# Performance work log

Measured on AMD Instinct MI355X. Metric: run time of the kernel, lower is better.

Reference implementation:

```python
import jax, jax.numpy as jnp
import numpy as np
from jax import lax

DIM = 1024
INNER = 2048  # dim * expand_factor
STATE = 64
B, T = 4, 2048
DECAY = 0.95
INPUT_FACTOR = 0.05
LN_EPS = 1e-5


def setup_inputs() -> dict:
    key = jax.random.key(0)
    ks = jax.random.split(key, 8)
    s = 0.02  # small weight scale
    return {
        "x": jax.random.normal(ks[0], (B, T, DIM), jnp.float32),
        "W_in": jax.random.normal(ks[1], (2 * INNER, DIM), jnp.float32) * s,
        "conv_w": jax.random.normal(ks[2], (INNER, 1, 4), jnp.float32) * s,
        "conv_b": jax.random.normal(ks[3], (INNER,), jnp.float32) * s,
        "W_B": jax.random.normal(ks[4], (STATE, INNER), jnp.float32) * s,
        "W_C": jax.random.normal(ks[5], (INNER, STATE), jnp.float32) * s,
        "D_param": jax.random.normal(ks[6], (INNER,), jnp.float32) * s,
        "W_out": jax.random.normal(ks[7], (DIM, INNER), jnp.float32) * s,
        "ln_gamma": jnp.ones((DIM,), jnp.float32),
        "ln_beta": jnp.zeros((DIM,), jnp.float32),
    }


def _layernorm(x, g, b):
    mu = jnp.mean(x, axis=-1, keepdims=True)
    var = jnp.mean(jnp.square(x - mu), axis=-1, keepdims=True)
    return (x - mu) * lax.rsqrt(var + LN_EPS) * g + b


def reference(x, W_in, conv_w, conv_b, W_B, W_C, D_param, W_out, ln_gamma, ln_beta):
    Bn, Tn, Dn = x.shape
    # in_proj -> split into input/gate halves
    x_proj = jnp.einsum("btd,ed->bte", x, W_in)  # [B,T,2*INNER]
    x_input, x_gate = jnp.split(x_proj, 2, axis=-1)
    # depthwise causal conv1d (torch pad=3 then slice [:T] == left-pad 3)
    xc = lax.conv_general_dilated(
        x_input.transpose(0, 2, 1),  # [B,C,T]
        conv_w,                       # [C,1,4]
        window_strides=(1,),
        padding=[(3, 0)],
        feature_group_count=INNER,
    ) + conv_b[None, :, None]
    u = jax.nn.silu(xc).transpose(0, 2, 1)  # [B,T,INNER]
    # linear recurrence: h_t = 0.95*h_{t-1} + 0.05*B_proj(u_t); h_0 = 0
    Bu = jnp.einsum("btc,sc->bts", u, W_B)  # [B,T,STATE]

    def step(h, bu_t):
        h = DECAY * h + INPUT_FACTOR * bu_t
        return h, h

    h0 = jnp.zeros((Bn, STATE), x.dtype)
    _, hs = lax.scan(step, h0, Bu.transpose(1, 0, 2))  # hs: [T,B,STATE]
    hs = hs.transpose(1, 0, 2)  # [B,T,STATE]
    y = jnp.einsum("bts,cs->btc", hs, W_C) + D_param * u  # [B,T,INNER]
    y = y * jax.nn.silu(x_gate)
    y = jnp.einsum("btc,dc->btd", y, W_out)  # [B,T,DIM]
    return _layernorm(y + x, ln_gamma, ln_beta)
```

## Files before the change

kernel.cpp:

```cpp
#include <hip/hip_runtime.h>
#include <hip/hip_bf16.h>

#define T_SEQ 2048
#define DIMD  1024
#define INNER 2048
#define STATE 64
#define BATCH 4
#define NCHUNK 64
#define CHUNK_L (T_SEQ / NCHUNK)
#define MROWS (BATCH * T_SEQ)
#define PSTRIDE ((long)MROWS * STATE)

typedef __hip_bfloat16 bf16;
typedef __attribute__((ext_vector_type(8))) short bf16x8v;
typedef __attribute__((ext_vector_type(4))) float f32x4v;
typedef __attribute__((ext_vector_type(4))) short short4v;

__device__ __forceinline__ float b2f(short s) {
    unsigned u = ((unsigned)(unsigned short)s) << 16;
    float f;
    __builtin_memcpy(&f, &u, 4);
    return f;
}
__device__ __forceinline__ short f2b(float f) {
    bf16 h = __float2bfloat16(f);
    short s;
    __builtin_memcpy(&s, &h, 2);
    return s;
}

__device__ __forceinline__ void gld_lds16(void* lds, const void* gsrc) {
    __builtin_amdgcn_global_load_lds(
        (const __attribute__((address_space(1))) unsigned*)gsrc,
        (__attribute__((address_space(3))) unsigned*)lds, 16, 0, 0);
}

template<int N> __device__ __forceinline__ void waitcnt_vm() {
    if constexpr (N == 8)      asm volatile("s_waitcnt vmcnt(8)" ::: "memory");
    else if constexpr (N == 4) asm volatile("s_waitcnt vmcnt(4)" ::: "memory");
    else                       asm volatile("s_waitcnt vmcnt(0)" ::: "memory");
}
__device__ __forceinline__ void block_barrier() {
    asm volatile("" ::: "memory");
    __builtin_amdgcn_s_barrier();
    asm volatile("" ::: "memory");
}

template<int BM, int BN, int BK, int WR, int WC, int EPI, int SPLITK>
__global__ __launch_bounds__(WR*WC*64, 2)
void gemm_ring(const short* __restrict__ A, const short* __restrict__ B,
               void* __restrict__ Cout, int M, int N, int K,
               const short* __restrict__ u_ptr, const short* __restrict__ gate_ptr,
               const float* __restrict__ Dp)
{
    constexpr int MFR = BM / (WR * 16);
    constexpr int NFR = BN / (WC * 16);
    constexpr int THREADS = WR * WC * 64;
    constexpr int UPR = BK / 8;
    constexpr int AISS = (BM * UPR) / THREADS;
    constexpr int BISS = (BN * UPR) / THREADS;
    constexpr int LPS  = AISS + BISS;
    __shared__ __align__(16) short As[2][BM * BK];
    __shared__ __align__(16) short Bs[2][BN * BK];

    const int tid  = threadIdx.x;
    const int lane = tid & 63;
    const int wave = tid >> 6;
    const int wm = (wave / WC) * (MFR * 16);
    const int wn = (wave % WC) * (NFR * 16);
    const long bm = (long)blockIdx.y * BM;
    const long bn = (long)blockIdx.x * BN;

    f32x4v acc[MFR][NFR];
#pragma unroll
    for (int m = 0; m < MFR; m++)
#pragma unroll
        for (int n = 0; n < NFR; n++)
            acc[m][n] = (f32x4v){0.f, 0.f, 0.f, 0.f};

    const int rsel = lane & 15;
    const int ssrc = (((tid & 7) ^ ((tid >> 3) & 7)) * 8);
    const int swz  = lane & 7;

    int kbeg = 0, kend = K;
    if constexpr (SPLITK > 1) {
        const int kch = K / SPLITK;
        kbeg = blockIdx.z * kch;
        kend = kbeg + kch;
    }
    const int nt = (kend - kbeg) / BK;

    auto stage = [&](int buf, int k0) {
#pragma unroll
        for (int i = 0; i < AISS; i++) {
            const int j = i * THREADS + tid;
            gld_lds16(&As[buf][j * 8],
                      &A[(bm + (j >> 3)) * (long)K + k0 + ssrc]);
        }
#pragma unroll
        for (int i = 0; i < BISS; i++) {
            const int j = i * THREADS + tid;
            gld_lds16(&Bs[buf][j * 8],
                      &B[(bn + (j >> 3)) * (long)K + k0 + ssrc]);
        }
    };
    auto compute = [&](int buf) {
#pragma unroll
        for (int kk = 0; kk < BK; kk += 32) {
            const int slog = (kk >> 3) + (lane >> 4);
            const int soff = ((slog ^ swz) * 8);
            bf16x8v af[MFR], bfv[NFR];
#pragma unroll
            for (int m = 0; m < MFR; m++)
                af[m] = *(const bf16x8v*)&As[buf][(wm + m * 16 + rsel) * BK + soff];
#pragma unroll
            for (int n = 0; n < NFR; n++)
                bfv[n] = *(const bf16x8v*)&Bs[buf][(wn + n * 16 + rsel) * BK + soff];
#pragma unroll
            for (int m = 0; m < MFR; m++)
#pragma unroll
                for (int n = 0; n < NFR; n++)
                    acc[m][n] = __builtin_amdgcn_mfma_f32_16x16x32_bf16(
                        af[m], bfv[n], acc[m][n], 0, 0, 0);
        }
    };

    stage(0, kbeg);
    for (int t = 0; t < nt; ++t) {
        const bool pf = (t + 1 < nt);
        if (pf) stage((t + 1) & 1, kbeg + (t + 1) * BK);
        if (pf) waitcnt_vm<LPS>();
        else    waitcnt_vm<0>();
        block_barrier();
        compute(t & 1);
        block_barrier();
    }

    float* fout = (float*)Cout;
    if constexpr (SPLITK > 1)
        fout += (long)blockIdx.z * (long)M * N;

#pragma unroll
    for (int m = 0; m < MFR; m++) {
#pragma unroll
        for (int n = 0; n < NFR; n++) {
            const long col  = bn + wn + n * 16 + (lane & 15);
            const long row0 = bm + wm + m * 16 + (lane >> 4) * 4;
#pragma unroll
            for (int j = 0; j < 4; j++) {
                const long row = row0 + j;
                const float v = acc[m][n][j];
                const long idx = row * (long)N + col;
                if constexpr (EPI == 0) {
                    ((short*)Cout)[idx] = f2b(v);
                } else if constexpr (EPI == 1) {
                    fout[idx] = v;
                } else {
                    float uv = b2f(u_ptr[row * (long)INNER + col]);
                    float gv = b2f(gate_ptr[row * (long)(2 * INNER) + col]);
                    float yv = v + Dp[col] * uv;
                    float sg = gv / (1.f + __expf(-gv));
                    ((short*)Cout)[idx] = f2b(yv * sg);
                }
            }
        }
    }
}

__global__ __launch_bounds__(256)
void conv_silu_kernel(const short* __restrict__ xproj, const float* __restrict__ cw,
                      const float* __restrict__ cb, short* __restrict__ u)
{
    const int bt = blockIdx.x;
    const int t  = bt & (T_SEQ - 1);
    const int c0 = threadIdx.x * 8;

    float wreg[4][8];
#pragma unroll
    for (int i = 0; i < 8; i++) {
        float4 wv = *(const float4*)&cw[(c0 + i) * 4];
        wreg[0][i] = wv.x; wreg[1][i] = wv.y; wreg[2][i] = wv.z; wreg[3][i] = wv.w;
    }
    float acc[8];
#pragma unroll
    for (int i = 0; i < 8; i++) acc[i] = cb[c0 + i];

#pragma unroll
    for (int k = 0; k < 4; k++) {
        if (t - 3 + k < 0) continue;
        bf16x8v v = *(const bf16x8v*)&xproj[(long)(bt - 3 + k) * (2 * INNER) + c0];
#pragma unroll
        for (int i = 0; i < 8; i++) acc[i] += b2f(v[i]) * wreg[k][i];
    }
    short o[8];
#pragma unroll
    for (int i = 0; i < 8; i++) {
        float s = acc[i] / (1.f + __expf(-acc[i]));
        o[i] = f2b(s);
    }
    *(bf16x8v*)&u[(long)bt * INNER + c0] = *(const bf16x8v*)o;
}

__global__ __launch_bounds__(64)
void scan_local_kernel(const float* __restrict__ Bu, float* __restrict__ locfin)
{
    const int b  = blockIdx.x / NCHUNK;
    const int ch = blockIdx.x % NCHUNK;
    const long base = ((long)b * T_SEQ + (long)ch * CHUNK_L) * STATE + threadIdx.x;
    float h = 0.f;
#pragma unroll
    for (int t = 0; t < CHUNK_L; t++) {
        const long o = base + (long)t * STATE;
        float bu = (Bu[o] + Bu[o + PSTRIDE]) + (Bu[o + 2 * PSTRIDE] + Bu[o + 3 * PSTRIDE]);
        h = 0.95f * h + 0.05f * bu;
    }
    locfin[(long)blockIdx.x * STATE + threadIdx.x] = h;
}

__global__ __launch_bounds__(256)
void carry_kernel(const float* __restrict__ locfin, float* __restrict__ carry,
                  float decayL)
{
    __shared__ float sm[BATCH * NCHUNK * STATE];
    for (int i = threadIdx.x; i < BATCH * NCHUNK * STATE; i += 256)
        sm[i] = locfin[i];
    __syncthreads();
    const int b = threadIdx.x >> 6, s = threadIdx.x & 63;
    float c = 0.f;
    for (int ch = 0; ch < NCHUNK; ch++) {
        const int idx = (b * NCHUNK + ch) * STATE + s;
        carry[idx] = c;
        c = decayL * c + sm[idx];
    }
}

__global__ __launch_bounds__(64)
void scan_apply_kernel(const float* __restrict__ Bu, const float* __restrict__ carry,
                       short* __restrict__ hs)
{
    const int b  = blockIdx.x / NCHUNK;
    const int ch = blockIdx.x % NCHUNK;
    const long base = ((long)b * T_SEQ + (long)ch * CHUNK_L) * STATE + threadIdx.x;
    float h = carry[(long)blockIdx.x * STATE + threadIdx.x];
#pragma unroll
    for (int t = 0; t < CHUNK_L; t++) {
        const long o = base + (long)t * STATE;
        float bu = (Bu[o] + Bu[o + PSTRIDE]) + (Bu[o + 2 * PSTRIDE] + Bu[o + 3 * PSTRIDE]);
        h = 0.95f * h + 0.05f * bu;
        hs[o] = f2b(h);
    }
}

__global__ __launch_bounds__(256)
void ln_kernel(const float* __restrict__ yo, const float* __restrict__ x,
               const float* __restrict__ g, const float* __restrict__ b,
               float* __restrict__ out)
{
    const int row = blockIdx.x;
    const int c   = threadIdx.x * 4;
    const long off = (long)row * DIMD + c;
    float4 yv = *(const float4*)&yo[off];
    float4 xv = *(const float4*)&x[off];
    float s0 = yv.x + xv.x, s1 = yv.y + xv.y, s2 = yv.z + xv.z, s3 = yv.w + xv.w;
    float sum = s0 + s1 + s2 + s3;
    float sq  = s0 * s0 + s1 * s1 + s2 * s2 + s3 * s3;
#pragma unroll
    for (int o = 32; o > 0; o >>= 1) {
        sum += __shfl_down(sum, o);
        sq  += __shfl_down(sq, o);
    }
    __shared__ float rs[4], rq[4];
    const int wave = threadIdx.x >> 6, lane = threadIdx.x & 63;
    if (lane == 0) { rs[wave] = sum; rq[wave] = sq; }
    __syncthreads();
    float tsum = rs[0] + rs[1] + rs[2] + rs[3];
    float tsq  = rq[0] + rq[1] + rq[2] + rq[3];
    float mu  = tsum * (1.f / DIMD);
    float inv = rsqrtf(tsq * (1.f / DIMD) - mu * mu + 1e-5f);
    float4 gv = *(const float4*)&g[c];
    float4 bv = *(const float4*)&b[c];
    float4 ov;
    ov.x = (s0 - mu) * inv * gv.x + bv.x;
    ov.y = (s1 - mu) * inv * gv.y + bv.y;
    ov.z = (s2 - mu) * inv * gv.z + bv.z;
    ov.w = (s3 - mu) * inv * gv.w + bv.w;
    *(float4*)&out[off] = ov;
}

#define C4_X   2097152L
#define C4_W1  (C4_X + 1048576L)
#define C4_WB  (C4_W1 + 32768L)
#define C4_WC  (C4_WB + 32768L)
#define C4_TOT (C4_WC + 524288L)

__global__ __launch_bounds__(256)
void cvt5_kernel(const float* __restrict__ x, const float* __restrict__ w1,
                 const float* __restrict__ wB, const float* __restrict__ wC,
                 const float* __restrict__ wO, short* __restrict__ dst)
{
    const long i = (long)blockIdx.x * 256 + threadIdx.x;
    if (i >= C4_TOT) return;
    const float* s;
    long off;
    if      (i < C4_X)  { s = x;  off = i; }
    else if (i < C4_W1) { s = w1; off = i - C4_X; }
    else if (i < C4_WB) { s = wB; off = i - C4_W1; }
    else if (i < C4_WC) { s = wC; off = i - C4_WB; }
    else                { s = wO; off = i - C4_WC; }
    float4 v = *(const float4*)&s[off * 4];
    short4v o = { f2b(v.x), f2b(v.y), f2b(v.z), f2b(v.w) };
    *(short4v*)&dst[i * 4] = o;
}

extern "C" void kernel_launch(void* const* d_in, const int* in_sizes, int n_in,
                              void* d_out, int out_size, void* d_ws, size_t ws_size,
                              hipStream_t stream)
{
    const float* x     = (const float*)d_in[0];
    const float* W_in  = (const float*)d_in[1];
    const float* cw    = (const float*)d_in[2];
    const float* cb    = (const float*)d_in[3];
    const float* W_B   = (const float*)d_in[4];
    const float* W_C   = (const float*)d_in[5];
    const float* Dp    = (const float*)d_in[6];
    const float* W_out = (const float*)d_in[7];
    const float* ln_g  = (const float*)d_in[8];
    const float* ln_b  = (const float*)d_in[9];

    char* p = (char*)d_ws;
    short* xw    = (short*)(p);
    short* w1    = (short*)(p +  16777216);
    short* wB    = (short*)(p +  25165824);
    short* wC    = (short*)(p +  25427968);
    short* wO    = (short*)(p +  25690112);
    short* xproj = (short*)(p +  29884416);
    short* u     = (short*)(p +  96993280);
    short* hs    = (short*)(p + 132644864);
    short* yg    = u;
    float* yout  = (float*)(p + 29884416);
    float* locfin = (float*)(p);
    float* carry  = (float*)(p + 65536);
    float* BuP    = (float*)(p + 131072);

    const int M = MROWS;

    cvt5_kernel<<<(int)((C4_TOT + 255) / 256), 256, 0, stream>>>(
        x, W_in, W_B, W_C, W_out, xw);

    gemm_ring<256, 256, 64, 2, 4, 0, 1><<<dim3(2 * INNER / 256, M / 256), 512, 0, stream>>>(
        xw, w1, xproj, M, 2 * INNER, DIMD, nullptr, nullptr, nullptr);

    conv_silu_kernel<<<M, 256, 0, stream>>>(xproj, cw, cb, u);

    gemm_ring<64, 64, 64, 2, 2, 1, 4><<<dim3(1, M / 64, 4), 256, 0, stream>>>(
        u, wB, BuP, M, STATE, INNER, nullptr, nullptr, nullptr);

    float decayL;
    {
        double dd = 1.0;
        for (int i = 0; i < CHUNK_L; i++) dd *= 0.95;
        decayL = (float)dd;
    }
    scan_local_kernel<<<BATCH * NCHUNK, STATE, 0, stream>>>(BuP, locfin);
    carry_kernel<<<1, 256, 0, stream>>>(locfin, carry, decayL);
    scan_apply_kernel<<<BATCH * NCHUNK, STATE, 0, stream>>>(BuP, carry, hs);

    gemm_ring<128, 128, 64, 2, 2, 2, 1><<<dim3(INNER / 128, M / 128), 256, 0, stream>>>(
        hs, wC, yg, M, INNER, STATE, u, xproj + INNER, Dp);

    gemm_ring<128, 128, 64, 2, 2, 1, 1><<<dim3(DIMD / 128, M / 128), 256, 0, stream>>>(
        yg, wO, yout, M, DIMD, INNER, nullptr, nullptr, nullptr);

    ln_kernel<<<M, 256, 0, stream>>>(yout, x, ln_g, ln_b, (float*)d_out);
}
```

Before: 255.7 us.

## Fuse residual add into out-proj epilogue, store bf16, add XCD block swizzle

The output-projection GEMM gains a new epilogue that adds the bf16-converted input x and writes a bf16 result. LayerNorm then reads one bf16 tensor instead of two fp32 tensors, which cuts the memory traffic of that kernel and of the GEMM store. Several GEMMs also get a block-index remap that spreads consecutive workgroups across the 8 XCDs for better L2 locality. The residual is now taken from the bf16 copy of x and the pre-LN sum is stored in bf16, which lowers precision.

Measured after the change: 243.7 us. -4.7%, faster.

```diff
diff --git a/kernel.cpp b/kernel.cpp
--- a/kernel.cpp
+++ b/kernel.cpp
@@ -46,7 +46,7 @@
     asm volatile("" ::: "memory");
 }
 
-template<int BM, int BN, int BK, int WR, int WC, int EPI, int SPLITK>
+template<int BM, int BN, int BK, int WR, int WC, int EPI, int SPLITK, int XSWZ>
 __global__ __launch_bounds__(WR*WC*64, 2)
 void gemm_ring(const short* __restrict__ A, const short* __restrict__ B,
                void* __restrict__ Cout, int M, int N, int K,
@@ -63,13 +63,23 @@
     __shared__ __align__(16) short As[2][BM * BK];
     __shared__ __align__(16) short Bs[2][BN * BK];
 
+    int bx = blockIdx.x, by = blockIdx.y;
+    if constexpr (XSWZ) {
+        const int gx = gridDim.x;
+        const int nwg = gx * gridDim.y;
+        int id = by * gx + bx;
+        const int cpx = nwg >> 3;
+        id = (id & 7) * cpx + (id >> 3);
+        bx = id % gx; by = id / gx;
+    }
+
     const int tid  = threadIdx.x;
     const int lane = tid & 63;
     const int wave = tid >> 6;
     const int wm = (wave / WC) * (MFR * 16);
     const int wn = (wave % WC) * (NFR * 16);
-    const long bm = (long)blockIdx.y * BM;
-    const long bn = (long)blockIdx.x * BN;
+    const long bm = (long)by * BM;
+    const long bn = (long)bx * BN;
 
     f32x4v acc[MFR][NFR];
 #pragma unroll
@@ -155,12 +165,14 @@
                     ((short*)Cout)[idx] = f2b(v);
                 } else if constexpr (EPI == 1) {
                     fout[idx] = v;
-                } else {
+                } else if constexpr (EPI == 2) {
                     float uv = b2f(u_ptr[row * (long)INNER + col]);
                     float gv = b2f(gate_ptr[row * (long)(2 * INNER) + col]);
                     float yv = v + Dp[col] * uv;
                     float sg = gv / (1.f + __expf(-gv));
                     ((short*)Cout)[idx] = f2b(yv * sg);
+                } else {
+                    ((short*)Cout)[idx] = f2b(v + b2f(u_ptr[idx]));
                 }
             }
         }
@@ -252,16 +264,14 @@
 }
 
 __global__ __launch_bounds__(256)
-void ln_kernel(const float* __restrict__ yo, const float* __restrict__ x,
-               const float* __restrict__ g, const float* __restrict__ b,
-               float* __restrict__ out)
+void ln_kernel(const short* __restrict__ yx, const float* __restrict__ g,
+               const float* __restrict__ b, float* __restrict__ out)
 {
     const int row = blockIdx.x;
     const int c   = threadIdx.x * 4;
     const long off = (long)row * DIMD + c;
-    float4 yv = *(const float4*)&yo[off];
-    float4 xv = *(const float4*)&x[off];
-    float s0 = yv.x + xv.x, s1 = yv.y + xv.y, s2 = yv.z + xv.z, s3 = yv.w + xv.w;
+    const short4v yv = *(const short4v*)&yx[off];
+    float s0 = b2f(yv[0]), s1 = b2f(yv[1]), s2 = b2f(yv[2]), s3 = b2f(yv[3]);
     float sum = s0 + s1 + s2 + s3;
     float sq  = s0 * s0 + s1 * s1 + s2 * s2 + s3 * s3;
 #pragma unroll
@@ -337,22 +347,22 @@
     short* u     = (short*)(p +  96993280);
     short* hs    = (short*)(p + 132644864);
     short* yg    = u;
-    float* yout  = (float*)(p + 29884416);
-    float* locfin = (float*)(p);
-    float* carry  = (float*)(p + 65536);
-    float* BuP    = (float*)(p + 131072);
+    short* yx    = xproj;
+    float* BuP    = (float*)(p + 16777216);
+    float* locfin = (float*)(p + 25165824);
+    float* carry  = (float*)(p + 25231360);
 
     const int M = MROWS;
 
     cvt5_kernel<<<(int)((C4_TOT + 255) / 256), 256, 0, stream>>>(
         x, W_in, W_B, W_C, W_out, xw);
 
-    gemm_ring<256, 256, 64, 2, 4, 0, 1><<<dim3(2 * INNER / 256, M / 256), 512, 0, stream>>>(
+    gemm_ring<256, 256, 64, 2, 4, 0, 1, 1><<<dim3(2 * INNER / 256, M / 256), 512, 0, stream>>>(
         xw, w1, xproj, M, 2 * INNER, DIMD, nullptr, nullptr, nullptr);
 
     conv_silu_kernel<<<M, 256, 0, stream>>>(xproj, cw, cb, u);
 
-    gemm_ring<64, 64, 64, 2, 2, 1, 4><<<dim3(1, M / 64, 4), 256, 0, stream>>>(
+    gemm_ring<64, 64, 64, 2, 2, 1, 4, 0><<<dim3(1, M / 64, 4), 256, 0, stream>>>(
         u, wB, BuP, M, STATE, INNER, nullptr, nullptr, nullptr);
 
     float decayL;
@@ -365,11 +375,11 @@
     carry_kernel<<<1, 256, 0, stream>>>(locfin, carry, decayL);
     scan_apply_kernel<<<BATCH * NCHUNK, STATE, 0, stream>>>(BuP, carry, hs);
 
-    gemm_ring<128, 128, 64, 2, 2, 2, 1><<<dim3(INNER / 128, M / 128), 256, 0, stream>>>(
+    gemm_ring<128, 128, 64, 2, 2, 2, 1, 1><<<dim3(INNER / 128, M / 128), 256, 0, stream>>>(
         hs, wC, yg, M, INNER, STATE, u, xproj + INNER, Dp);
 
-    gemm_ring<128, 128, 64, 2, 2, 1, 1><<<dim3(DIMD / 128, M / 128), 256, 0, stream>>>(
-        yg, wO, yout, M, DIMD, INNER, nullptr, nullptr, nullptr);
-
-    ln_kernel<<<M, 256, 0, stream>>>(yout, x, ln_g, ln_b, (float*)d_out);
-}
+    gemm_ring<128, 128, 64, 2, 2, 3, 1, 1><<<dim3(DIMD / 128, M / 128), 256, 0, stream>>>(
+        yg, wO, yx, M, DIMD, INNER, xw, nullptr, nullptr);
+
+    ln_kernel<<<M, 256, 0, stream>>>(yx, ln_g, ln_b, (float*)d_out);
+}
```
